# Performance work log

Measured on AMD Instinct MI355X. Metric: run time of the kernel, lower is better.

The kernel has to match this reference:

```python
import jax, jax.numpy as jnp
import numpy as np


def gcn_layer(x, src, dst, W, b, n_dst):
    # DGL GraphConv, norm='both': D_src^{-1/2} pre-norm, sum aggregate, D_dst^{-1/2} post-norm, + bias
    n_src = x.shape[0]
    e_ones = jnp.ones(src.shape[0], dtype=x.dtype)
    deg_out = jnp.clip(jax.ops.segment_sum(e_ones, src, num_segments=n_src), 1.0)
    deg_in = jnp.clip(jax.ops.segment_sum(e_ones, dst, num_segments=n_dst), 1.0)
    h = (x * jax.lax.rsqrt(deg_out)[:, None]) @ W          # [n_src, out]
    agg = jax.ops.segment_sum(h[src], dst, num_segments=n_dst)  # [n_dst, out]
    return jax.nn.relu(agg * jax.lax.rsqrt(deg_in)[:, None] + b)


def setup_inputs() -> dict:
    key = jax.random.key(0)
    ks = jax.random.split(key, 8)
    N_SRC0, N_DST0, N_DST1 = 400000, 40000, 4000
    E0, E1 = 400000, 40000
    D_IN, D_HID, D_OUT = 256, 256, 256
    x = jax.random.normal(ks[0], (N_SRC0, D_IN), dtype=jnp.float32)
    src0 = jax.random.randint(ks[1], (E0,), 0, N_SRC0)
    dst0 = jax.random.randint(ks[2], (E0,), 0, N_DST0)
    src1 = jax.random.randint(ks[3], (E1,), 0, N_DST0)
    dst1 = jax.random.randint(ks[4], (E1,), 0, N_DST1)
    W0 = jax.random.normal(ks[5], (D_IN, D_HID), dtype=jnp.float32) * (1.0 / np.sqrt(D_IN))
    W1 = jax.random.normal(ks[6], (D_HID, D_OUT), dtype=jnp.float32) * (1.0 / np.sqrt(D_HID))
    b0 = jnp.zeros((D_HID,), dtype=jnp.float32)
    b1 = jnp.zeros((D_OUT,), dtype=jnp.float32)
    return {"x": x, "src0": src0, "dst0": dst0, "src1": src1, "dst1": dst1,
            "W0": W0, "b0": b0, "W1": W1, "b1": b1,
            "n_dst0": N_DST0, "n_dst1": N_DST1}


def reference(x, src0, dst0, src1, dst1, W0, b0, W1, b1, n_dst0, n_dst1):
    h = gcn_layer(x, src0, dst0, W0, b0, n_dst0)   # [n_dst0, hidden]
    out = gcn_layer(h, src1, dst1, W1, b1, n_dst1)  # [n_dst1, out]
    return out
```

## Files before the change

### kernel.cpp

```cpp
#include <hip/hip_runtime.h>
#include <hip/hip_bf16.h>
#include <cstddef>
#include <cstdint>


#define D 256
#define N_DST0_CONST 40000

typedef __attribute__((ext_vector_type(8))) short s16x8;
typedef __attribute__((ext_vector_type(4))) short s16x4;
typedef __attribute__((ext_vector_type(4))) float f32x4;

__device__ inline short f2bf(float f) {
    __hip_bfloat16 h = __float2bfloat16(f);
    return *reinterpret_cast<short*>(&h);
}

__global__ void zero_i(int* __restrict__ p, int n) {
    int i = blockIdx.x * blockDim.x + threadIdx.x;
    int stride = gridDim.x * blockDim.x;
    for (; i < n; i += stride) p[i] = 0;
}

__global__ void count_deg_both(const int* __restrict__ src0, const int* __restrict__ dst0, int E0,
                               const int* __restrict__ src1, const int* __restrict__ dst1, int E1,
                               int* __restrict__ cs0, int* __restrict__ cd0,
                               int* __restrict__ cs1, int* __restrict__ cd1) {
    int e = blockIdx.x * blockDim.x + threadIdx.x;
    if (e < E0) {
        atomicAdd(&cs0[src0[e]], 1);
        atomicAdd(&cd0[dst0[e]], 1);
    } else if (e < E0 + E1) {
        int i = e - E0;
        atomicAdd(&cs1[src1[i]], 1);
        atomicAdd(&cd1[dst1[i]], 1);
    }
}

__global__ __launch_bounds__(1024) void ex_scan_both(
    const int* __restrict__ cnt0, int* __restrict__ ptr0, int n0,
    const int* __restrict__ cnt1, int* __restrict__ ptr1, int n1) {
    const int* cnt = (blockIdx.x == 0) ? cnt0 : cnt1;
    int* ptr = (blockIdx.x == 0) ? ptr0 : ptr1;
    int n = (blockIdx.x == 0) ? n0 : n1;

    __shared__ int wsum[16];
    const int tid = threadIdx.x;
    const int chunk = (n + 1023) / 1024;
    const int begin = min(tid * chunk, n);
    const int end = min(begin + chunk, n);
    int local = 0;
    for (int i = begin; i < end; ++i) local += cnt[i];
    const int lane = tid & 63;
    const int wid = tid >> 6;
    int v = local;
    for (int off = 1; off < 64; off <<= 1) {
        int u = __shfl_up(v, off, 64);
        if (lane >= off) v += u;
    }
    if (lane == 63) wsum[wid] = v;
    __syncthreads();
    if (wid == 0 && lane < 16) {
        int w = wsum[lane];
        for (int off = 1; off < 16; off <<= 1) {
            int u = __shfl_up(w, off, 16);
            if (lane >= off) w += u;
        }
        wsum[lane] = w;
    }
    __syncthreads();
    int base = (wid > 0 ? wsum[wid - 1] : 0) + (v - local);
    int run = base;
    for (int i = begin; i < end; ++i) { ptr[i] = run; run += cnt[i]; }
}

__global__ void fill_csr_both(const int* __restrict__ src0, const int* __restrict__ dst0, int E0,
                              const int* __restrict__ src1, const int* __restrict__ dst1, int E1,
                              int* __restrict__ ptr0, int* __restrict__ es0,
                              int* __restrict__ ptr1, int* __restrict__ es1) {
    int e = blockIdx.x * blockDim.x + threadIdx.x;
    if (e < E0) {
        int pos = atomicAdd(&ptr0[dst0[e]], 1);
        es0[pos] = src0[e];
    } else if (e < E0 + E1) {
        int i = e - E0;
        int pos = atomicAdd(&ptr1[dst1[i]], 1);
        es1[pos] = src1[i];
    }
}

__global__ __launch_bounds__(256) void gather_agg_bf16(
    const float* __restrict__ X, const int* __restrict__ edge_src,
    const int* __restrict__ ptr, const int* __restrict__ cnt_src,
    short* __restrict__ agg, int nrows) {
    int d = blockIdx.x * 4 + threadIdx.y;
    if (d >= nrows) return;
    int beg = (d == 0) ? 0 : ptr[d - 1];
    int end = ptr[d];
    int deg = end - beg;
    int lane = threadIdx.x;

    int s_l = 0;
    float rn_l = 0.f;
    if (lane < deg) {
        s_l = edge_src[beg + lane];
        rn_l = rsqrtf(fmaxf((float)cnt_src[s_l], 1.0f));
    }

    float4 acc = make_float4(0.f, 0.f, 0.f, 0.f);
    int nb = min(deg, 64);
    int j = 0;
    for (; j + 4 <= nb; j += 4) {
        int s0 = __shfl(s_l, j + 0), s1 = __shfl(s_l, j + 1);
        int s2 = __shfl(s_l, j + 2), s3 = __shfl(s_l, j + 3);
        float r0 = __shfl(rn_l, j + 0), r1 = __shfl(rn_l, j + 1);
        float r2 = __shfl(rn_l, j + 2), r3 = __shfl(rn_l, j + 3);
        float4 v0 = *(const float4*)(X + (size_t)s0 * D + lane * 4);
        float4 v1 = *(const float4*)(X + (size_t)s1 * D + lane * 4);
        float4 v2 = *(const float4*)(X + (size_t)s2 * D + lane * 4);
        float4 v3 = *(const float4*)(X + (size_t)s3 * D + lane * 4);
        acc.x += v0.x * r0 + v1.x * r1 + v2.x * r2 + v3.x * r3;
        acc.y += v0.y * r0 + v1.y * r1 + v2.y * r2 + v3.y * r3;
        acc.z += v0.z * r0 + v1.z * r1 + v2.z * r2 + v3.z * r3;
        acc.w += v0.w * r0 + v1.w * r1 + v2.w * r2 + v3.w * r3;
    }
    for (; j < nb; ++j) {
        int s = __shfl(s_l, j);
        float r = __shfl(rn_l, j);
        float4 v = *(const float4*)(X + (size_t)s * D + lane * 4);
        acc.x += v.x * r; acc.y += v.y * r; acc.z += v.z * r; acc.w += v.w * r;
    }
    for (int jj = beg + 64; jj < end; ++jj) {
        int s = edge_src[jj];
        float r = rsqrtf(fmaxf((float)cnt_src[s], 1.0f));
        float4 v = *(const float4*)(X + (size_t)s * D + lane * 4);
        acc.x += v.x * r; acc.y += v.y * r; acc.z += v.z * r; acc.w += v.w * r;
    }

    s16x4 o;
    o.x = f2bf(acc.x); o.y = f2bf(acc.y); o.z = f2bf(acc.z); o.w = f2bf(acc.w);
    *(s16x4*)(agg + (size_t)d * D + lane * 4) = o;
}

__global__ __launch_bounds__(256) void transpose_cast_w_both(
    const float* __restrict__ Wa, short* __restrict__ BTa,
    const float* __restrict__ Wb, short* __restrict__ BTb) {
    const float* W = (blockIdx.z == 0) ? Wa : Wb;
    short* BT = (blockIdx.z == 0) ? BTa : BTb;
    __shared__ float t[16][17];
    int k0 = blockIdx.x * 16, n0 = blockIdx.y * 16;
    t[threadIdx.y][threadIdx.x] = W[(size_t)(k0 + threadIdx.y) * D + n0 + threadIdx.x];
    __syncthreads();
    BT[(size_t)(n0 + threadIdx.y) * D + k0 + threadIdx.x] = f2bf(t[threadIdx.x][threadIdx.y]);
}

#define LDK 40

__global__ __launch_bounds__(256) void gemm_bf16_mfma(
    const short* __restrict__ A, const short* __restrict__ BT,
    const int* __restrict__ cnt_dst, const float* __restrict__ bias,
    float* __restrict__ out, int M) {
    __shared__ short As[128][LDK];
    __shared__ short Bs[128][LDK];

    const int tid = threadIdx.x;
    const int m0 = blockIdx.x * 128;
    const int n0 = blockIdx.y * 128;
    const int wave = tid >> 6;
    const int lane = tid & 63;
    const int l15 = lane & 15;
    const int quad = lane >> 4;
    const int mo = (wave & 1) * 64;
    const int no = (wave >> 1) * 64;

    f32x4 acc[4][4] = {};

    for (int k0 = 0; k0 < D; k0 += 32) {
#pragma unroll
        for (int i = 0; i < 2; ++i) {
            int idx = tid + i * 256;
            int row = idx >> 2;
            int kg = (idx & 3) * 8;
            int gm = m0 + row;
            s16x8 av = {};
            if (gm < M) av = *(const s16x8*)(A + (size_t)gm * D + k0 + kg);
            *(s16x8*)&As[row][kg] = av;
            s16x8 bv = *(const s16x8*)(BT + (size_t)(n0 + row) * D + k0 + kg);
            *(s16x8*)&Bs[row][kg] = bv;
        }
        __syncthreads();

        s16x8 af[4], bf[4];
#pragma unroll
        for (int mt = 0; mt < 4; ++mt)
            af[mt] = *(const s16x8*)&As[mo + mt * 16 + l15][quad * 8];
#pragma unroll
        for (int nt = 0; nt < 4; ++nt)
            bf[nt] = *(const s16x8*)&Bs[no + nt * 16 + l15][quad * 8];
#pragma unroll
        for (int mt = 0; mt < 4; ++mt)
#pragma unroll
            for (int nt = 0; nt < 4; ++nt)
                acc[mt][nt] = __builtin_amdgcn_mfma_f32_16x16x32_bf16(
                    af[mt], bf[nt], acc[mt][nt], 0, 0, 0);
        __syncthreads();
    }

#pragma unroll
    for (int mt = 0; mt < 4; ++mt) {
#pragma unroll
        for (int r = 0; r < 4; ++r) {
            int gm = m0 + mo + mt * 16 + quad * 4 + r;
            if (gm >= M) continue;
            float sc = rsqrtf(fmaxf((float)cnt_dst[gm], 1.0f));
#pragma unroll
            for (int nt = 0; nt < 4; ++nt) {
                int gn = n0 + no + nt * 16 + l15;
                float v = fmaxf(acc[mt][nt][r] * sc + bias[gn], 0.f);
                out[(size_t)gm * D + gn] = v;
            }
        }
    }
}


extern "C" void kernel_launch(void* const* d_in, const int* in_sizes, int n_in,
                              void* d_out, int out_size, void* d_ws, size_t ws_size,
                              hipStream_t stream) {
    const float* x    = (const float*)d_in[0];
    const int*   src0 = (const int*)d_in[1];
    const int*   dst0 = (const int*)d_in[2];
    const int*   src1 = (const int*)d_in[3];
    const int*   dst1 = (const int*)d_in[4];
    const float* W0   = (const float*)d_in[5];
    const float* b0   = (const float*)d_in[6];
    const float* W1   = (const float*)d_in[7];
    const float* b1   = (const float*)d_in[8];

    const int n_src0 = in_sizes[0] / D;
    const int E0     = in_sizes[1];
    const int E1     = in_sizes[3];
    const int n_dst0 = N_DST0_CONST;
    const int n_dst1 = out_size / D;

    char* base = (char*)d_ws;
    size_t off = 0;
    auto alloc = [&](size_t bytes) { void* p = base + off; off = (off + bytes + 63) & ~(size_t)63; return p; };

    int* icnt = (int*)alloc((size_t)(n_src0 + 2 * n_dst0 + n_dst1) * 4);
    int* icnt_src0 = icnt;
    int* icnt_dst0 = icnt + n_src0;
    int* icnt_src1 = icnt + n_src0 + n_dst0;
    int* icnt_dst1 = icnt + n_src0 + 2 * n_dst0;
    const int cnt_total = n_src0 + 2 * n_dst0 + n_dst1;

    int* ptr0      = (int*)alloc((size_t)n_dst0 * 4);
    int* ptr1      = (int*)alloc((size_t)n_dst1 * 4);
    int* edge_src0 = (int*)alloc((size_t)E0 * 4);
    int* edge_src1 = (int*)alloc((size_t)E1 * 4);

    float* h0    = (float*)alloc((size_t)n_dst0 * D * 4);
    short* aggb0 = (short*)alloc((size_t)n_dst0 * D * 2);
    short* aggb1 = (short*)alloc((size_t)n_dst1 * D * 2);
    short* BT0   = (short*)alloc((size_t)D * D * 2);
    short* BT1   = (short*)alloc((size_t)D * D * 2);

    float* out = (float*)d_out;

    zero_i<<<512, 256, 0, stream>>>(icnt, cnt_total);

    count_deg_both<<<(E0 + E1 + 255) / 256, 256, 0, stream>>>(
        src0, dst0, E0, src1, dst1, E1, icnt_src0, icnt_dst0, icnt_src1, icnt_dst1);

    ex_scan_both<<<2, 1024, 0, stream>>>(icnt_dst0, ptr0, n_dst0, icnt_dst1, ptr1, n_dst1);

    fill_csr_both<<<(E0 + E1 + 255) / 256, 256, 0, stream>>>(
        src0, dst0, E0, src1, dst1, E1, ptr0, edge_src0, ptr1, edge_src1);

    {
        dim3 g(D / 16, D / 16, 2), b(16, 16);
        transpose_cast_w_both<<<g, b, 0, stream>>>(W0, BT0, W1, BT1);
    }

    {
        dim3 blk(64, 4);
        gather_agg_bf16<<<(n_dst0 + 3) / 4, blk, 0, stream>>>(x, edge_src0, ptr0, icnt_src0, aggb0, n_dst0);
        dim3 grid((n_dst0 + 127) / 128, D / 128);
        gemm_bf16_mfma<<<grid, 256, 0, stream>>>(aggb0, BT0, icnt_dst0, b0, h0, n_dst0);
    }

    {
        dim3 blk(64, 4);
        gather_agg_bf16<<<(n_dst1 + 3) / 4, blk, 0, stream>>>(h0, edge_src1, ptr1, icnt_src1, aggb1, n_dst1);
        dim3 grid((n_dst1 + 127) / 128, D / 128);
        gemm_bf16_mfma<<<grid, 256, 0, stream>>>(aggb1, BT1, icnt_dst1, b1, out, n_dst1);
    }
}
```

Before: 697.1 us.

## Pre-scale and cast source features to bf16 before gather-sum

Adds a pass that multiplies each source row by its out-degree rsqrt and stores it as bf16. The gather kernels then sum bf16 rows without per-edge normalization, halving the bytes per gathered row. The first GEMM's epilogue now writes the hidden layer directly as bf16, pre-scaled by the next layer's source-degree norm. In exchange, the new cast pass streams the full 400k-row input once (rows with zero out-degree are skipped), and source features are rounded to bf16 before aggregation.

```diff
diff --git a/kernel.cpp b/kernel.cpp
--- a/kernel.cpp
+++ b/kernel.cpp
@@ -14,6 +14,10 @@
 __device__ inline short f2bf(float f) {
     __hip_bfloat16 h = __float2bfloat16(f);
     return *reinterpret_cast<short*>(&h);
+}
+__device__ inline float bf2f(short h) {
+    unsigned u = ((unsigned)(unsigned short)h) << 16;
+    return __uint_as_float(u);
 }
 
 __global__ void zero_i(int* __restrict__ p, int n) {
@@ -89,10 +93,25 @@
     }
 }
 
-__global__ __launch_bounds__(256) void gather_agg_bf16(
-    const float* __restrict__ X, const int* __restrict__ edge_src,
-    const int* __restrict__ ptr, const int* __restrict__ cnt_src,
-    short* __restrict__ agg, int nrows) {
+__global__ __launch_bounds__(256) void scale_cast_rows(
+    const float* __restrict__ X, const int* __restrict__ cnt,
+    short* __restrict__ XB, int nrows) {
+    int r = blockIdx.x * 4 + threadIdx.y;
+    if (r >= nrows) return;
+    int c = cnt[r];
+    if (c == 0) return;
+    float sc = rsqrtf((float)c);
+    int lane = threadIdx.x;
+    float4 v = *(const float4*)(X + (size_t)r * D + lane * 4);
+    s16x4 o;
+    o.x = f2bf(v.x * sc); o.y = f2bf(v.y * sc);
+    o.z = f2bf(v.z * sc); o.w = f2bf(v.w * sc);
+    *(s16x4*)(XB + (size_t)r * D + lane * 4) = o;
+}
+
+__global__ __launch_bounds__(256) void gather_sum_bf16(
+    const short* __restrict__ XB, const int* __restrict__ edge_src,
+    const int* __restrict__ ptr, short* __restrict__ agg, int nrows) {
     int d = blockIdx.x * 4 + threadIdx.y;
     if (d >= nrows) return;
     int beg = (d == 0) ? 0 : ptr[d - 1];
@@ -100,45 +119,36 @@
     int deg = end - beg;
     int lane = threadIdx.x;
 
-    int s_l = 0;
-    float rn_l = 0.f;
-    if (lane < deg) {
-        s_l = edge_src[beg + lane];
-        rn_l = rsqrtf(fmaxf((float)cnt_src[s_l], 1.0f));
-    }
-
-    float4 acc = make_float4(0.f, 0.f, 0.f, 0.f);
+    int s_l = (lane < deg) ? edge_src[beg + lane] : 0;
+
+    float ax = 0.f, ay = 0.f, az = 0.f, aw = 0.f;
     int nb = min(deg, 64);
     int j = 0;
     for (; j + 4 <= nb; j += 4) {
         int s0 = __shfl(s_l, j + 0), s1 = __shfl(s_l, j + 1);
         int s2 = __shfl(s_l, j + 2), s3 = __shfl(s_l, j + 3);
-        float r0 = __shfl(rn_l, j + 0), r1 = __shfl(rn_l, j + 1);
-        float r2 = __shfl(rn_l, j + 2), r3 = __shfl(rn_l, j + 3);
-        float4 v0 = *(const float4*)(X + (size_t)s0 * D + lane * 4);
-        float4 v1 = *(const float4*)(X + (size_t)s1 * D + lane * 4);
-        float4 v2 = *(const float4*)(X + (size_t)s2 * D + lane * 4);
-        float4 v3 = *(const float4*)(X + (size_t)s3 * D + lane * 4);
-        acc.x += v0.x * r0 + v1.x * r1 + v2.x * r2 + v3.x * r3;
-        acc.y += v0.y * r0 + v1.y * r1 + v2.y * r2 + v3.y * r3;
-        acc.z += v0.z * r0 + v1.z * r1 + v2.z * r2 + v3.z * r3;
-        acc.w += v0.w * r0 + v1.w * r1 + v2.w * r2 + v3.w * r3;
+        s16x4 v0 = *(const s16x4*)(XB + (size_t)s0 * D + lane * 4);
+        s16x4 v1 = *(const s16x4*)(XB + (size_t)s1 * D + lane * 4);
+        s16x4 v2 = *(const s16x4*)(XB + (size_t)s2 * D + lane * 4);
+        s16x4 v3 = *(const s16x4*)(XB + (size_t)s3 * D + lane * 4);
+        ax += bf2f(v0.x) + bf2f(v1.x) + bf2f(v2.x) + bf2f(v3.x);
+        ay += bf2f(v0.y) + bf2f(v1.y) + bf2f(v2.y) + bf2f(v3.y);
+        az += bf2f(v0.z) + bf2f(v1.z) + bf2f(v2.z) + bf2f(v3.z);
+        aw += bf2f(v0.w) + bf2f(v1.w) + bf2f(v2.w) + bf2f(v3.w);
     }
     for (; j < nb; ++j) {
         int s = __shfl(s_l, j);
-        float r = __shfl(rn_l, j);
-        float4 v = *(const float4*)(X + (size_t)s * D + lane * 4);
-        acc.x += v.x * r; acc.y += v.y * r; acc.z += v.z * r; acc.w += v.w * r;
+        s16x4 v = *(const s16x4*)(XB + (size_t)s * D + lane * 4);
+        ax += bf2f(v.x); ay += bf2f(v.y); az += bf2f(v.z); aw += bf2f(v.w);
     }
     for (int jj = beg + 64; jj < end; ++jj) {
         int s = edge_src[jj];
-        float r = rsqrtf(fmaxf((float)cnt_src[s], 1.0f));
-        float4 v = *(const float4*)(X + (size_t)s * D + lane * 4);
-        acc.x += v.x * r; acc.y += v.y * r; acc.z += v.z * r; acc.w += v.w * r;
+        s16x4 v = *(const s16x4*)(XB + (size_t)s * D + lane * 4);
+        ax += bf2f(v.x); ay += bf2f(v.y); az += bf2f(v.z); aw += bf2f(v.w);
     }
 
     s16x4 o;
-    o.x = f2bf(acc.x); o.y = f2bf(acc.y); o.z = f2bf(acc.z); o.w = f2bf(acc.w);
+    o.x = f2bf(ax); o.y = f2bf(ay); o.z = f2bf(az); o.w = f2bf(aw);
     *(s16x4*)(agg + (size_t)d * D + lane * 4) = o;
 }
 
@@ -159,7 +169,8 @@
 __global__ __launch_bounds__(256) void gemm_bf16_mfma(
     const short* __restrict__ A, const short* __restrict__ BT,
     const int* __restrict__ cnt_dst, const float* __restrict__ bias,
-    float* __restrict__ out, int M) {
+    float* __restrict__ out_f, short* __restrict__ out_b,
+    const int* __restrict__ cnt_next, int mode, int M) {
     __shared__ short As[128][LDK];
     __shared__ short Bs[128][LDK];
 
@@ -213,11 +224,14 @@
             int gm = m0 + mo + mt * 16 + quad * 4 + r;
             if (gm >= M) continue;
             float sc = rsqrtf(fmaxf((float)cnt_dst[gm], 1.0f));
+            float sc2 = 1.0f;
+            if (mode == 1) sc2 = rsqrtf(fmaxf((float)cnt_next[gm], 1.0f));
 #pragma unroll
             for (int nt = 0; nt < 4; ++nt) {
                 int gn = n0 + no + nt * 16 + l15;
                 float v = fmaxf(acc[mt][nt][r] * sc + bias[gn], 0.f);
-                out[(size_t)gm * D + gn] = v;
+                if (mode == 1) out_b[(size_t)gm * D + gn] = f2bf(v * sc2);
+                else           out_f[(size_t)gm * D + gn] = v;
             }
         }
     }
@@ -259,7 +273,8 @@
     int* edge_src0 = (int*)alloc((size_t)E0 * 4);
     int* edge_src1 = (int*)alloc((size_t)E1 * 4);
 
-    float* h0    = (float*)alloc((size_t)n_dst0 * D * 4);
+    short* xb    = (short*)alloc((size_t)n_src0 * D * 2);
+    short* h0b   = (short*)alloc((size_t)n_dst0 * D * 2);
     short* aggb0 = (short*)alloc((size_t)n_dst0 * D * 2);
     short* aggb1 = (short*)alloc((size_t)n_dst1 * D * 2);
     short* BT0   = (short*)alloc((size_t)D * D * 2);
@@ -284,15 +299,22 @@
 
     {
         dim3 blk(64, 4);
-        gather_agg_bf16<<<(n_dst0 + 3) / 4, blk, 0, stream>>>(x, edge_src0, ptr0, icnt_src0, aggb0, n_dst0);
-        dim3 grid((n_dst0 + 127) / 128, D / 128);
-        gemm_bf16_mfma<<<grid, 256, 0, stream>>>(aggb0, BT0, icnt_dst0, b0, h0, n_dst0);
+        scale_cast_rows<<<(n_src0 + 3) / 4, blk, 0, stream>>>(x, icnt_src0, xb, n_src0);
     }
 
     {
         dim3 blk(64, 4);
-        gather_agg_bf16<<<(n_dst1 + 3) / 4, blk, 0, stream>>>(h0, edge_src1, ptr1, icnt_src1, aggb1, n_dst1);
+        gather_sum_bf16<<<(n_dst0 + 3) / 4, blk, 0, stream>>>(xb, edge_src0, ptr0, aggb0, n_dst0);
+        dim3 grid((n_dst0 + 127) / 128, D / 128);
+        gemm_bf16_mfma<<<grid, 256, 0, stream>>>(aggb0, BT0, icnt_dst0, b0,
+                                                 nullptr, h0b, icnt_src1, 1, n_dst0);
+    }
+
+    {
+        dim3 blk(64, 4);
+        gather_sum_bf16<<<(n_dst1 + 3) / 4, blk, 0, stream>>>(h0b, edge_src1, ptr1, aggb1, n_dst1);
         dim3 grid((n_dst1 + 127) / 128, D / 128);
-        gemm_bf16_mfma<<<grid, 256, 0, stream>>>(aggb1, BT1, icnt_dst1, b1, out, n_dst1);
-    }
-}
+        gemm_bf16_mfma<<<grid, 256, 0, stream>>>(aggb1, BT1, icnt_dst1, b1,
+                                                 out, nullptr, nullptr, 0, n_dst1);
+    }
+}
```

New measurement: 746.1 us. 1.07x slower.
